# Kernel optimization log

Measured on AMD Instinct MI355X. Metric: run time of the kernel, lower is better.

## Reference

```python
import jax, jax.numpy as jnp
import numpy as np

EMBED_DIM = 512
FFN_DIM = 2048
N_QUBITS = 8
BATCH = 16
SEQ = 2048


def setup_inputs() -> dict:
    key = jax.random.key(0)
    k_x, k_t, k_w1, k_w2 = jax.random.split(key, 4)
    x = jax.random.normal(k_x, (BATCH, SEQ, EMBED_DIM), dtype=jnp.float32)
    # per-wire trainable RX angles (nn.Parameter(torch.randn(1)) per qubit)
    theta = jax.random.normal(k_t, (N_QUBITS,), dtype=jnp.float32)
    # nn.Linear weights, bias=False; stored as [out, in] like torch
    s1 = 1.0 / np.sqrt(N_QUBITS)
    s2 = 1.0 / np.sqrt(FFN_DIM)
    W1 = jax.random.uniform(k_w1, (FFN_DIM, N_QUBITS), jnp.float32, -s1, s1)
    W2 = jax.random.uniform(k_w2, (EMBED_DIM, FFN_DIM), jnp.float32, -s2, s2)
    return {"x": x, "theta": theta, "W1": W1, "W2": W2}


def reference(x, theta, W1, W2):
    # Quantum circuit closed form: each wire i gets RX(x_i) twice (outer loop
    # + encoder) plus trainable RX(theta_i); product state => <Z_i> = cos(total angle).
    q = jnp.cos(2.0 * x[..., :N_QUBITS] + theta)          # [B, S, n_qubits]
    # dropout in eval mode is identity
    h = jax.nn.relu(jnp.einsum('bsq,fq->bsf', q, W1))     # [B, S, ffn_dim]
    out = jnp.einsum('bsf,ef->bse', h, W2)                # [B, S, embed_dim]
    return out
```

## Files before the change

### kernel.cpp

```cpp
#include <hip/hip_runtime.h>
#include <cstdint>

#define BATCH 16
#define SEQ 2048
#define EMB 512
#define FFN 2048
#define NQ 8
#define M_TOTAL (BATCH * SEQ)

#define BM 128
#define BN 256
#define BK 32
#define NTHREADS 512

typedef __attribute__((ext_vector_type(8))) short short8;
typedef __attribute__((ext_vector_type(4))) float float4v;
typedef __attribute__((ext_vector_type(4))) unsigned int uint4v;

static __device__ __forceinline__ unsigned int f2bf(float f) {
    unsigned int u = __builtin_bit_cast(unsigned int, f);
    return (u + 0x7fffu + ((u >> 16) & 1u)) >> 16;
}
static __device__ __forceinline__ unsigned int f2bf_pk(float lo, float hi) {
    return f2bf(lo) | (f2bf(hi) << 16);
}

__global__ __launch_bounds__(256) void prep_w2(const float* __restrict__ W2,
                                               unsigned int* __restrict__ w2b) {
    int idx = (blockIdx.x * 256 + threadIdx.x) * 4;
    float4 v = *(const float4*)&W2[idx];
    w2b[idx / 2]     = f2bf_pk(v.x, v.y);
    w2b[idx / 2 + 1] = f2bf_pk(v.z, v.w);
}


__global__ __launch_bounds__(NTHREADS, 4) void ffq_main(
    const float* __restrict__ x,
    const float* __restrict__ theta,
    const float* __restrict__ W1,
    const unsigned short* __restrict__ w2b,
    float* __restrict__ out)
{
    __shared__ unsigned short Asm[2][BM * BK];
    __shared__ unsigned short Bsm[2][BN * BK];
    __shared__ unsigned short w1s[FFN * NQ];

    const int t    = threadIdx.x;
    const int m0   = blockIdx.x * BM;
    const int n0   = blockIdx.y * BN;
    const int wave = t >> 6, lane = t & 63;
    const int quad = lane >> 4, l16 = lane & 15;
    const int wm   = wave >> 2, wn = wave & 3;

#pragma unroll
    for (int i = 0; i < (FFN * NQ / 2) / NTHREADS; ++i) {
        int p = i * NTHREADS + t;
        float2 v = *(const float2*)&W1[p * 2];
        *(unsigned int*)&w1s[p * 2] = f2bf_pk(v.x, v.y);
    }

    short8 qfrag;
    {
        int qrow = m0 + wave * 16 + l16;
        const float* xr = x + (size_t)qrow * EMB;
        float4 xa = *(const float4*)xr;
        float4 xb = *(const float4*)(xr + 4);
        uint4v uq;
        uq[0] = f2bf_pk(__cosf(2.f * xa.x + theta[0]), __cosf(2.f * xa.y + theta[1]));
        uq[1] = f2bf_pk(__cosf(2.f * xa.z + theta[2]), __cosf(2.f * xa.w + theta[3]));
        uq[2] = f2bf_pk(__cosf(2.f * xb.x + theta[4]), __cosf(2.f * xb.y + theta[5]));
        uq[3] = f2bf_pk(__cosf(2.f * xb.z + theta[6]), __cosf(2.f * xb.w + theta[7]));
        qfrag = __builtin_bit_cast(short8, uq);
        if (quad != 0) qfrag = (short8)0;
    }

    const int c0 = t, c1 = NTHREADS + t;
    const int n0c0 = c0 >> 2, s0c = c0 & 3;
    const int n0c1 = c1 >> 2, s1c = c1 & 3;
    const unsigned short* gB0 =
        w2b + (size_t)(n0 + n0c0) * FFN + (s0c ^ ((n0c0 >> 1) & 3)) * 8;
    const unsigned short* gB1 =
        w2b + (size_t)(n0 + n0c1) * FFN + (s1c ^ ((n0c1 >> 1) & 3)) * 8;

    auto stageB = [&](int k0, int buf) __attribute__((always_inline)) {
        __builtin_amdgcn_global_load_lds(
            (const __attribute__((address_space(1))) unsigned int*)(gB0 + k0),
            (__attribute__((address_space(3))) unsigned int*)(uintptr_t)(&Bsm[buf][c0 * 8]),
            16, 0, 0);
        __builtin_amdgcn_global_load_lds(
            (const __attribute__((address_space(1))) unsigned int*)(gB1 + k0),
            (__attribute__((address_space(3))) unsigned int*)(uintptr_t)(&Bsm[buf][c1 * 8]),
            16, 0, 0);
    };

    const int hm   = wave * 16 + l16;
    const int hswz = (l16 >> 1) & 3;
    auto hgen = [&](int kh, int buf) __attribute__((always_inline)) {
#pragma unroll
        for (int fh = 0; fh < 2; ++fh) {
            int f = kh + fh * 16 + l16;
            short8 w1f = *(const short8*)&w1s[f * NQ];
            float4v hc = __builtin_amdgcn_mfma_f32_16x16x32_bf16(
                w1f, qfrag, (float4v)0.0f, 0, 0, 0);
            unsigned int p0 = f2bf_pk(fmaxf(hc[0], 0.f), fmaxf(hc[1], 0.f));
            unsigned int p1 = f2bf_pk(fmaxf(hc[2], 0.f), fmaxf(hc[3], 0.f));
            int qph = (fh * 2 + (quad >> 1)) ^ hswz;
            unsigned long long pk = ((unsigned long long)p1 << 32) | p0;
            *(unsigned long long*)&Asm[buf][hm * 32 + qph * 8 + (quad & 1) * 4] = pk;
        }
    };

    float4v acc[16];
#pragma unroll
    for (int i = 0; i < 16; ++i) acc[i] = (float4v)0.0f;

    auto compute = [&](int buf) __attribute__((always_inline)) {
        short8 af[4], bfr[4];
#pragma unroll
        for (int fm = 0; fm < 4; ++fm) {
            int row = wm * 64 + fm * 16 + l16;
            int qph = quad ^ ((row >> 1) & 3);
            af[fm] = *(const short8*)&Asm[buf][row * 32 + qph * 8];
        }
#pragma unroll
        for (int fn = 0; fn < 4; ++fn) {
            int row = wn * 64 + fn * 16 + l16;
            int qph = quad ^ ((row >> 1) & 3);
            bfr[fn] = *(const short8*)&Bsm[buf][row * 32 + qph * 8];
        }
#pragma unroll
        for (int fm = 0; fm < 4; ++fm)
#pragma unroll
            for (int fn = 0; fn < 4; ++fn)
                acc[fm * 4 + fn] = __builtin_amdgcn_mfma_f32_16x16x32_bf16(
                    af[fm], bfr[fn], acc[fm * 4 + fn], 0, 0, 0);
    };

    __syncthreads();
    stageB(0, 0);
    hgen(0, 0);
    __syncthreads();

    for (int kt = 0; kt < 62; kt += 2) {
        stageB((kt + 1) * BK, 1);
        hgen((kt + 1) * BK, 1);
        compute(0);
        __syncthreads();

        stageB((kt + 2) * BK, 0);
        hgen((kt + 2) * BK, 0);
        compute(1);
        __syncthreads();
    }
    stageB(63 * BK, 1);
    hgen(63 * BK, 1);
    compute(0);
    __syncthreads();
    compute(1);

    const int om = m0 + wm * 64;
    const int on = n0 + wn * 64;
#pragma unroll
    for (int fm = 0; fm < 4; ++fm) {
#pragma unroll
        for (int fn = 0; fn < 4; ++fn) {
            float4v v = acc[fm * 4 + fn];
            int rbase = om + fm * 16 + quad * 4;
            int c     = on + fn * 16 + l16;
#pragma unroll
            for (int r = 0; r < 4; ++r)
                out[(size_t)(rbase + r) * EMB + c] = v[r];
        }
    }
}

extern "C" void kernel_launch(void* const* d_in, const int* in_sizes, int n_in,
                              void* d_out, int out_size, void* d_ws, size_t ws_size,
                              hipStream_t stream) {
    const float* x     = (const float*)d_in[0];
    const float* theta = (const float*)d_in[1];
    const float* W1    = (const float*)d_in[2];
    const float* W2    = (const float*)d_in[3];
    float* out = (float*)d_out;

    unsigned int* w2b = (unsigned int*)d_ws;

    prep_w2<<<(EMB * FFN) / (256 * 4), 256, 0, stream>>>(W2, w2b);

    dim3 grid(M_TOTAL / BM, EMB / BN);
    ffq_main<<<grid, NTHREADS, 0, stream>>>(x, theta, W1, (const unsigned short*)w2b, out);
}
```

Baseline: 172.9 us.

## Double M tile to 256 rows per block with 128x64 warp tiles

```diff
diff --git a/kernel.cpp b/kernel.cpp
--- a/kernel.cpp
+++ b/kernel.cpp
@@ -8,7 +8,7 @@
 #define NQ 8
 #define M_TOTAL (BATCH * SEQ)
 
-#define BM 128
+#define BM 256
 #define BN 256
 #define BK 32
 #define NTHREADS 512
@@ -34,7 +34,7 @@
 }
 
 
-__global__ __launch_bounds__(NTHREADS, 4) void ffq_main(
+__global__ __launch_bounds__(NTHREADS, 2) void ffq_main(
     const float* __restrict__ x,
     const float* __restrict__ theta,
     const float* __restrict__ W1,
@@ -59,9 +59,10 @@
         *(unsigned int*)&w1s[p * 2] = f2bf_pk(v.x, v.y);
     }
 
-    short8 qfrag;
-    {
-        int qrow = m0 + wave * 16 + l16;
+    short8 qfrag[2];
+#pragma unroll
+    for (int g2 = 0; g2 < 2; ++g2) {
+        int qrow = m0 + wave * 32 + g2 * 16 + l16;
         const float* xr = x + (size_t)qrow * EMB;
         float4 xa = *(const float4*)xr;
         float4 xb = *(const float4*)(xr + 4);
@@ -70,8 +71,8 @@
         uq[1] = f2bf_pk(__cosf(2.f * xa.z + theta[2]), __cosf(2.f * xa.w + theta[3]));
         uq[2] = f2bf_pk(__cosf(2.f * xb.x + theta[4]), __cosf(2.f * xb.y + theta[5]));
         uq[3] = f2bf_pk(__cosf(2.f * xb.z + theta[6]), __cosf(2.f * xb.w + theta[7]));
-        qfrag = __builtin_bit_cast(short8, uq);
-        if (quad != 0) qfrag = (short8)0;
+        qfrag[g2] = __builtin_bit_cast(short8, uq);
+        if (quad != 0) qfrag[g2] = (short8)0;
     }
 
     const int c0 = t, c1 = NTHREADS + t;
@@ -93,47 +94,51 @@
             16, 0, 0);
     };
 
-    const int hm   = wave * 16 + l16;
     const int hswz = (l16 >> 1) & 3;
     auto hgen = [&](int kh, int buf) __attribute__((always_inline)) {
+        short8 w1f[2];
+        w1f[0] = *(const short8*)&w1s[(kh + l16) * NQ];
+        w1f[1] = *(const short8*)&w1s[(kh + 16 + l16) * NQ];
 #pragma unroll
-        for (int fh = 0; fh < 2; ++fh) {
-            int f = kh + fh * 16 + l16;
-            short8 w1f = *(const short8*)&w1s[f * NQ];
-            float4v hc = __builtin_amdgcn_mfma_f32_16x16x32_bf16(
-                w1f, qfrag, (float4v)0.0f, 0, 0, 0);
-            unsigned int p0 = f2bf_pk(fmaxf(hc[0], 0.f), fmaxf(hc[1], 0.f));
-            unsigned int p1 = f2bf_pk(fmaxf(hc[2], 0.f), fmaxf(hc[3], 0.f));
-            int qph = (fh * 2 + (quad >> 1)) ^ hswz;
-            unsigned long long pk = ((unsigned long long)p1 << 32) | p0;
-            *(unsigned long long*)&Asm[buf][hm * 32 + qph * 8 + (quad & 1) * 4] = pk;
+        for (int g2 = 0; g2 < 2; ++g2) {
+#pragma unroll
+            for (int fh = 0; fh < 2; ++fh) {
+                float4v hc = __builtin_amdgcn_mfma_f32_16x16x32_bf16(
+                    w1f[fh], qfrag[g2], (float4v)0.0f, 0, 0, 0);
+                unsigned int p0 = f2bf_pk(fmaxf(hc[0], 0.f), fmaxf(hc[1], 0.f));
+                unsigned int p1 = f2bf_pk(fmaxf(hc[2], 0.f), fmaxf(hc[3], 0.f));
+                int m    = wave * 32 + g2 * 16 + l16;
+                int qph  = (fh * 2 + (quad >> 1)) ^ hswz;
+                unsigned long long pk = ((unsigned long long)p1 << 32) | p0;
+                *(unsigned long long*)&Asm[buf][m * 32 + qph * 8 + (quad & 1) * 4] = pk;
+            }
         }
     };
 
-    float4v acc[16];
+    float4v acc[32];
 #pragma unroll
-    for (int i = 0; i < 16; ++i) acc[i] = (float4v)0.0f;
+    for (int i = 0; i < 32; ++i) acc[i] = (float4v)0.0f;
 
     auto compute = [&](int buf) __attribute__((always_inline)) {
-        short8 af[4], bfr[4];
-#pragma unroll
-        for (int fm = 0; fm < 4; ++fm) {
-            int row = wm * 64 + fm * 16 + l16;
-            int qph = quad ^ ((row >> 1) & 3);
-            af[fm] = *(const short8*)&Asm[buf][row * 32 + qph * 8];
-        }
+        short8 bfr[4];
 #pragma unroll
         for (int fn = 0; fn < 4; ++fn) {
             int row = wn * 64 + fn * 16 + l16;
             int qph = quad ^ ((row >> 1) & 3);
             bfr[fn] = *(const short8*)&Bsm[buf][row * 32 + qph * 8];
         }
+        __builtin_amdgcn_s_setprio(1);
 #pragma unroll
-        for (int fm = 0; fm < 4; ++fm)
+        for (int fm = 0; fm < 8; ++fm) {
+            int row = wm * 128 + fm * 16 + l16;
+            int qph = quad ^ ((row >> 1) & 3);
+            short8 af = *(const short8*)&Asm[buf][row * 32 + qph * 8];
 #pragma unroll
             for (int fn = 0; fn < 4; ++fn)
                 acc[fm * 4 + fn] = __builtin_amdgcn_mfma_f32_16x16x32_bf16(
-                    af[fm], bfr[fn], acc[fm * 4 + fn], 0, 0, 0);
+                    af, bfr[fn], acc[fm * 4 + fn], 0, 0, 0);
+        }
+        __builtin_amdgcn_s_setprio(0);
     };
 
     __syncthreads();
@@ -158,10 +163,10 @@
     __syncthreads();
     compute(1);
 
-    const int om = m0 + wm * 64;
+    const int om = m0 + wm * 128;
     const int on = n0 + wn * 64;
 #pragma unroll
-    for (int fm = 0; fm < 4; ++fm) {
+    for (int fm = 0; fm < 8; ++fm) {
 #pragma unroll
         for (int fn = 0; fn < 4; ++fn) {
             float4v v = acc[fm * 4 + fn];
```

New measurement: 178.7 us. 3.4% more time.

## Split K-step into two barrier phases with explicit waitcnt and setprio pipelining

Applied to the files above, without the earlier changes.

```diff
diff --git a/kernel.cpp b/kernel.cpp
--- a/kernel.cpp
+++ b/kernel.cpp
@@ -93,70 +93,113 @@
             16, 0, 0);
     };
 
+    const int hswz = (l16 >> 1) & 3;
     const int hm   = wave * 16 + l16;
-    const int hswz = (l16 >> 1) & 3;
-    auto hgen = [&](int kh, int buf) __attribute__((always_inline)) {
-#pragma unroll
-        for (int fh = 0; fh < 2; ++fh) {
-            int f = kh + fh * 16 + l16;
-            short8 w1f = *(const short8*)&w1s[f * NQ];
-            float4v hc = __builtin_amdgcn_mfma_f32_16x16x32_bf16(
-                w1f, qfrag, (float4v)0.0f, 0, 0, 0);
-            unsigned int p0 = f2bf_pk(fmaxf(hc[0], 0.f), fmaxf(hc[1], 0.f));
-            unsigned int p1 = f2bf_pk(fmaxf(hc[2], 0.f), fmaxf(hc[3], 0.f));
-            int qph = (fh * 2 + (quad >> 1)) ^ hswz;
-            unsigned long long pk = ((unsigned long long)p1 << 32) | p0;
-            *(unsigned long long*)&Asm[buf][hm * 32 + qph * 8 + (quad & 1) * 4] = pk;
-        }
+    auto hgenH = [&](int kh, int buf, int fh) __attribute__((always_inline)) {
+        int f = kh + fh * 16 + l16;
+        short8 w1f = *(const short8*)&w1s[f * NQ];
+        float4v hc = __builtin_amdgcn_mfma_f32_16x16x32_bf16(
+            w1f, qfrag, (float4v)0.0f, 0, 0, 0);
+        unsigned int p0 = f2bf_pk(fmaxf(hc[0], 0.f), fmaxf(hc[1], 0.f));
+        unsigned int p1 = f2bf_pk(fmaxf(hc[2], 0.f), fmaxf(hc[3], 0.f));
+        int qph = (fh * 2 + (quad >> 1)) ^ hswz;
+        unsigned long long pk = ((unsigned long long)p1 << 32) | p0;
+        *(unsigned long long*)&Asm[buf][hm * 32 + qph * 8 + (quad & 1) * 4] = pk;
     };
 
     float4v acc[16];
 #pragma unroll
     for (int i = 0; i < 16; ++i) acc[i] = (float4v)0.0f;
 
-    auto compute = [&](int buf) __attribute__((always_inline)) {
-        short8 af[4], bfr[4];
+    short8 af[4], bf01[2], bf23[2];
+
+    auto readAf = [&](int buf) __attribute__((always_inline)) {
 #pragma unroll
         for (int fm = 0; fm < 4; ++fm) {
             int row = wm * 64 + fm * 16 + l16;
             int qph = quad ^ ((row >> 1) & 3);
             af[fm] = *(const short8*)&Asm[buf][row * 32 + qph * 8];
         }
-#pragma unroll
-        for (int fn = 0; fn < 4; ++fn) {
+    };
+    auto readB01 = [&](int buf) __attribute__((always_inline)) {
+#pragma unroll
+        for (int fn = 0; fn < 2; ++fn) {
             int row = wn * 64 + fn * 16 + l16;
             int qph = quad ^ ((row >> 1) & 3);
-            bfr[fn] = *(const short8*)&Bsm[buf][row * 32 + qph * 8];
-        }
+            bf01[fn] = *(const short8*)&Bsm[buf][row * 32 + qph * 8];
+        }
+    };
+    auto readB23 = [&](int buf) __attribute__((always_inline)) {
+#pragma unroll
+        for (int fn = 0; fn < 2; ++fn) {
+            int row = wn * 64 + (fn + 2) * 16 + l16;
+            int qph = quad ^ ((row >> 1) & 3);
+            bf23[fn] = *(const short8*)&Bsm[buf][row * 32 + qph * 8];
+        }
+    };
+
+#define FENCE() asm volatile("" ::: "memory")
+#define BAR()   do { FENCE(); __builtin_amdgcn_s_barrier(); FENCE(); } while (0)
+#define LGKM0() do { asm volatile("s_waitcnt lgkmcnt(0)" ::: "memory"); \
+                     __builtin_amdgcn_sched_barrier(0); } while (0)
+
+    auto phaseX = [&](int tt, int cb, bool dostage, bool dohg, int vmode)
+        __attribute__((always_inline)) {
+        readAf(cb);
+        readB23(cb);
+        if (dohg) hgenH((tt + 1) * BK, 1 - cb, 0);
+        BAR();
+        LGKM0();
+        __builtin_amdgcn_s_setprio(1);
+        if (dostage) stageB((tt + 2) * BK, cb);
 #pragma unroll
         for (int fm = 0; fm < 4; ++fm)
 #pragma unroll
-            for (int fn = 0; fn < 4; ++fn)
+            for (int fn = 0; fn < 2; ++fn)
                 acc[fm * 4 + fn] = __builtin_amdgcn_mfma_f32_16x16x32_bf16(
-                    af[fm], bfr[fn], acc[fm * 4 + fn], 0, 0, 0);
-    };
-
-    __syncthreads();
+                    af[fm], bf01[fn], acc[fm * 4 + fn], 0, 0, 0);
+        if (vmode == 2)      asm volatile("s_waitcnt vmcnt(2)" ::: "memory");
+        else if (vmode == 0) asm volatile("s_waitcnt vmcnt(0)" ::: "memory");
+        __builtin_amdgcn_s_setprio(0);
+        BAR();
+    };
+    auto phaseY = [&](int tt, int cb, bool dord, bool dohg)
+        __attribute__((always_inline)) {
+        if (dord) readB01(1 - cb);
+        if (dohg) hgenH((tt + 1) * BK, 1 - cb, 1);
+        BAR();
+        LGKM0();
+        __builtin_amdgcn_s_setprio(1);
+#pragma unroll
+        for (int fm = 0; fm < 4; ++fm)
+#pragma unroll
+            for (int fn = 0; fn < 2; ++fn)
+                acc[fm * 4 + 2 + fn] = __builtin_amdgcn_mfma_f32_16x16x32_bf16(
+                    af[fm], bf23[fn], acc[fm * 4 + 2 + fn], 0, 0, 0);
+        __builtin_amdgcn_s_setprio(0);
+        BAR();
+    };
+
+    asm volatile("s_waitcnt lgkmcnt(0)" ::: "memory");
+    BAR();
     stageB(0, 0);
-    hgen(0, 0);
-    __syncthreads();
+    stageB(1 * BK, 1);
+    hgenH(0, 0, 0);
+    hgenH(0, 0, 1);
+    asm volatile("s_waitcnt vmcnt(0) lgkmcnt(0)" ::: "memory");
+    BAR();
+    readB01(0);
 
     for (int kt = 0; kt < 62; kt += 2) {
-        stageB((kt + 1) * BK, 1);
-        hgen((kt + 1) * BK, 1);
-        compute(0);
-        __syncthreads();
-
-        stageB((kt + 2) * BK, 0);
-        hgen((kt + 2) * BK, 0);
-        compute(1);
-        __syncthreads();
-    }
-    stageB(63 * BK, 1);
-    hgen(63 * BK, 1);
-    compute(0);
-    __syncthreads();
-    compute(1);
+        phaseX(kt,     0, true, true, 2);
+        phaseY(kt,     0, true, true);
+        phaseX(kt + 1, 1, true, true, 2);
+        phaseY(kt + 1, 1, true, true);
+    }
+    phaseX(62, 0, false, true, 0);
+    phaseY(62, 0, true,  true);
+    phaseX(63, 1, false, false, -1);
+    phaseY(63, 1, false, false);
 
     const int om = m0 + wm * 64;
     const int on = n0 + wn * 64;
```

Result: slower. 180.2 us (+4.3%).

## Preconvert W1 to bf16 globally, reorder hgen after MFMA, use hardware bf16 pack

Applied to the files above, without the earlier changes.

```diff
diff --git a/kernel.cpp b/kernel.cpp
--- a/kernel.cpp
+++ b/kernel.cpp
@@ -24,6 +24,11 @@
 static __device__ __forceinline__ unsigned int f2bf_pk(float lo, float hi) {
     return f2bf(lo) | (f2bf(hi) << 16);
 }
+static __device__ __forceinline__ unsigned int cvt_pk_bf16(float lo, float hi) {
+    unsigned int r;
+    asm("v_cvt_pk_bf16_f32 %0, %1, %2" : "=v"(r) : "v"(lo), "v"(hi));
+    return r;
+}
 
 __global__ __launch_bounds__(256) void prep_w2(const float* __restrict__ W2,
                                                unsigned int* __restrict__ w2b) {
@@ -37,13 +42,12 @@
 __global__ __launch_bounds__(NTHREADS, 4) void ffq_main(
     const float* __restrict__ x,
     const float* __restrict__ theta,
-    const float* __restrict__ W1,
+    const unsigned short* __restrict__ w1b,
     const unsigned short* __restrict__ w2b,
     float* __restrict__ out)
 {
     __shared__ unsigned short Asm[2][BM * BK];
     __shared__ unsigned short Bsm[2][BN * BK];
-    __shared__ unsigned short w1s[FFN * NQ];
 
     const int t    = threadIdx.x;
     const int m0   = blockIdx.x * BM;
@@ -51,13 +55,6 @@
     const int wave = t >> 6, lane = t & 63;
     const int quad = lane >> 4, l16 = lane & 15;
     const int wm   = wave >> 2, wn = wave & 3;
-
-#pragma unroll
-    for (int i = 0; i < (FFN * NQ / 2) / NTHREADS; ++i) {
-        int p = i * NTHREADS + t;
-        float2 v = *(const float2*)&W1[p * 2];
-        *(unsigned int*)&w1s[p * 2] = f2bf_pk(v.x, v.y);
-    }
 
     short8 qfrag;
     {
@@ -93,17 +90,20 @@
             16, 0, 0);
     };
 
+    auto loadW1 = [&](int kh, short8& a, short8& b) __attribute__((always_inline)) {
+        a = *(const short8*)&w1b[(size_t)(kh + l16) * NQ];
+        b = *(const short8*)&w1b[(size_t)(kh + 16 + l16) * NQ];
+    };
+
+    const int hswz = (l16 >> 1) & 3;
     const int hm   = wave * 16 + l16;
-    const int hswz = (l16 >> 1) & 3;
-    auto hgen = [&](int kh, int buf) __attribute__((always_inline)) {
+    auto hgen = [&](int buf, short8 w1f0, short8 w1f1) __attribute__((always_inline)) {
 #pragma unroll
         for (int fh = 0; fh < 2; ++fh) {
-            int f = kh + fh * 16 + l16;
-            short8 w1f = *(const short8*)&w1s[f * NQ];
             float4v hc = __builtin_amdgcn_mfma_f32_16x16x32_bf16(
-                w1f, qfrag, (float4v)0.0f, 0, 0, 0);
-            unsigned int p0 = f2bf_pk(fmaxf(hc[0], 0.f), fmaxf(hc[1], 0.f));
-            unsigned int p1 = f2bf_pk(fmaxf(hc[2], 0.f), fmaxf(hc[3], 0.f));
+                fh ? w1f1 : w1f0, qfrag, (float4v)0.0f, 0, 0, 0);
+            unsigned int p0 = cvt_pk_bf16(fmaxf(hc[0], 0.f), fmaxf(hc[1], 0.f));
+            unsigned int p1 = cvt_pk_bf16(fmaxf(hc[2], 0.f), fmaxf(hc[3], 0.f));
             int qph = (fh * 2 + (quad >> 1)) ^ hswz;
             unsigned long long pk = ((unsigned long long)p1 << 32) | p0;
             *(unsigned long long*)&Asm[buf][hm * 32 + qph * 8 + (quad & 1) * 4] = pk;
@@ -128,33 +128,49 @@
             int qph = quad ^ ((row >> 1) & 3);
             bfr[fn] = *(const short8*)&Bsm[buf][row * 32 + qph * 8];
         }
+        __builtin_amdgcn_s_setprio(1);
 #pragma unroll
         for (int fm = 0; fm < 4; ++fm)
 #pragma unroll
             for (int fn = 0; fn < 4; ++fn)
                 acc[fm * 4 + fn] = __builtin_amdgcn_mfma_f32_16x16x32_bf16(
                     af[fm], bfr[fn], acc[fm * 4 + fn], 0, 0, 0);
-    };
-
+        __builtin_amdgcn_s_setprio(0);
+    };
+
+    {
+        short8 w1f0, w1f1;
+        loadW1(0, w1f0, w1f1);
+        stageB(0, 0);
+        hgen(0, w1f0, w1f1);
+    }
     __syncthreads();
-    stageB(0, 0);
-    hgen(0, 0);
-    __syncthreads();
 
     for (int kt = 0; kt < 62; kt += 2) {
-        stageB((kt + 1) * BK, 1);
-        hgen((kt + 1) * BK, 1);
+        {
+            short8 w1f0, w1f1;
+            loadW1((kt + 1) * BK, w1f0, w1f1);
+            stageB((kt + 1) * BK, 1);
+            compute(0);
+            hgen(1, w1f0, w1f1);
+        }
+        __syncthreads();
+        {
+            short8 w1f0, w1f1;
+            loadW1((kt + 2) * BK, w1f0, w1f1);
+            stageB((kt + 2) * BK, 0);
+            compute(1);
+            hgen(0, w1f0, w1f1);
+        }
+        __syncthreads();
+    }
+    {
+        short8 w1f0, w1f1;
+        loadW1(63 * BK, w1f0, w1f1);
+        stageB(63 * BK, 1);
         compute(0);
-        __syncthreads();
-
-        stageB((kt + 2) * BK, 0);
-        hgen((kt + 2) * BK, 0);
-        compute(1);
-        __syncthreads();
-    }
-    stageB(63 * BK, 1);
-    hgen(63 * BK, 1);
-    compute(0);
+        hgen(1, w1f0, w1f1);
+    }
     __syncthreads();
     compute(1);
 
@@ -184,9 +200,13 @@
     float* out = (float*)d_out;
 
     unsigned int* w2b = (unsigned int*)d_ws;
+    unsigned int* w1b = (unsigned int*)((char*)d_ws + (size_t)EMB * FFN * 2);
 
     prep_w2<<<(EMB * FFN) / (256 * 4), 256, 0, stream>>>(W2, w2b);
+    prep_w2<<<(FFN * NQ) / (256 * 4), 256, 0, stream>>>(W1, w1b);
 
     dim3 grid(M_TOTAL / BM, EMB / BN);
-    ffq_main<<<grid, NTHREADS, 0, stream>>>(x, theta, W1, (const unsigned short*)w2b, out);
-}
+    ffq_main<<<grid, NTHREADS, 0, stream>>>(x, theta,
+                                            (const unsigned short*)w1b,
+                                            (const unsigned short*)w2b, out);
+}
```

Result: slower. 176.5 us (+2.1%).
